# Performance work log

Hardware: AMD Instinct MI355X
Metric: run time of the kernel (lower is better)

Reference implementation:

```python
import jax, jax.numpy as jnp
import numpy as np

B, S, D, H = 4, 2048, 768, 12
HD = D // H  # 64


def setup_inputs() -> dict:
    key = jax.random.key(0)
    ks = jax.random.split(key, 6)
    sc = 0.02
    return {
        "x": jax.random.normal(ks[0], (B, S, D), dtype=jnp.float32),
        "wq": jax.random.normal(ks[1], (D, D), dtype=jnp.float32) * sc,
        "wk": jax.random.normal(ks[2], (D, D), dtype=jnp.float32) * sc,
        "wv": jax.random.normal(ks[3], (D, D), dtype=jnp.float32) * sc,
        "wo": jax.random.normal(ks[4], (D, D), dtype=jnp.float32) * sc,
        "bo": jnp.zeros((D,), dtype=jnp.float32),
    }


def reference(x, wq, wk, wv, wo, bo):
    b, s, d = x.shape
    # nn.Linear applies x @ W^T; project then split heads -> [b, h, s, hd]
    def heads(w):
        return (x @ w.T).reshape(b, s, H, HD).transpose(0, 2, 1, 3)
    q, k, v = heads(wq), heads(wk), heads(wv)
    scores = jnp.einsum("bhqd,bhkd->bhqk", q, k)
    causal = jnp.triu(jnp.ones((s, s), dtype=bool), 1)
    # original masks with -inf BEFORE scaling; -inf/sqrt(d) == -inf, same softmax
    scores = jnp.where(causal, -jnp.inf, scores) / jnp.sqrt(jnp.float32(HD))
    attn = jax.nn.softmax(scores, axis=-1)  # dropout=0.0 (eval/deterministic)
    ctx = jnp.einsum("bhqk,bhkd->bhqd", attn, v)
    ctx = ctx.transpose(0, 2, 1, 3).reshape(b, s, d)
    return ctx @ wo.T + bo
```

## Files before the change

kernel.cpp:

```cpp
#include <hip/hip_runtime.h>

#define B_ 4
#define S_ 2048
#define D_ 768
#define H_ 12
#define HD_ 64
#define T_ (B_ * S_)

typedef __bf16 bf16x8 __attribute__((ext_vector_type(8)));
typedef __bf16 bf16x4 __attribute__((ext_vector_type(4)));
typedef float  f32x4  __attribute__((ext_vector_type(4)));

__device__ __forceinline__ f32x4 mfma16(bf16x8 a, bf16x8 b, f32x4 c) {
  return __builtin_amdgcn_mfma_f32_16x16x32_bf16(a, b, c, 0, 0, 0);
}

__device__ __forceinline__ float fexp2(float x) {
  float r;
  asm("v_exp_f32 %0, %1" : "=v"(r) : "v"(x));
  return r;
}

__device__ __forceinline__ void gload16(const __bf16* g, __bf16* lds) {
  __builtin_amdgcn_global_load_lds(
      (__attribute__((address_space(1))) void*)g,
      (__attribute__((address_space(3))) void*)lds, 16, 0, 0);
}

__global__ void cvt_all(const float* __restrict__ x,
                        const float* __restrict__ wq,
                        const float* __restrict__ wk,
                        const float* __restrict__ wv,
                        const float* __restrict__ wo,
                        __bf16* __restrict__ out) {
  constexpr int XN4 = T_ * D_ / 4;
  constexpr int WN4 = D_ * D_ / 4;
  const int i = blockIdx.x * blockDim.x + threadIdx.x;
  if (i >= XN4 + 4 * WN4) return;
  const float* src;
  int k;
  float scale = 1.0f;
  if (i < XN4) {
    src = x;
    k = i;
  } else {
    const int j = i - XN4;
    const int wsel = j / WN4;
    k = j - wsel * WN4;
    src = (wsel == 0) ? wq : (wsel == 1) ? wk : (wsel == 2) ? wv : wo;
    if (wsel == 1) scale = 0.18033688f;
  }
  const float4 v = reinterpret_cast<const float4*>(src)[k];
  bf16x4 o;
  o[0] = (__bf16)(v.x * scale);
  o[1] = (__bf16)(v.y * scale);
  o[2] = (__bf16)(v.z * scale);
  o[3] = (__bf16)(v.w * scale);
  reinterpret_cast<bf16x4*>(out)[i] = o;
}

template <int MODE>
__global__ __launch_bounds__(256)
__attribute__((amdgpu_waves_per_eu(2)))
void gemm_bt(const __bf16* __restrict__ A,
             const __bf16* __restrict__ W0, const __bf16* __restrict__ W1,
             const __bf16* __restrict__ W2,
             __bf16* __restrict__ Oq, __bf16* __restrict__ Ok,
             __bf16* __restrict__ Ov,
             float* __restrict__ fout, const float* __restrict__ bias) {
  constexpr int K = D_;
  constexpr int NT = K / 64;
  __shared__ __align__(16) char smem[65536];
  __bf16* sA0 = reinterpret_cast<__bf16*>(smem);
  __bf16* sB0 = reinterpret_cast<__bf16*>(smem + 32768);

  const int tid = threadIdx.x;
  const int l = tid & 63;
  const int w = tid >> 6;

  const int flat = blockIdx.y * 64 + blockIdx.x;
  const int xcd = flat & 7;
  const int q = flat >> 3;
  const int mtile = xcd * 8 + (q & 7);
  const int pan = q >> 3;
  const int m0 = mtile * 128;

  int mat, n0;
  const __bf16* Wm;
  if (MODE == 0) {
    mat = pan / 6;
    n0 = (pan % 6) * 128;
    Wm = (mat == 0) ? W0 : (mat == 1) ? W1 : W2;
  } else {
    mat = 0;
    n0 = pan * 128;
    Wm = W0;
  }

  const int srow = l >> 3;
  const int scol = ((l & 7) ^ srow) * 8;
  const __bf16* gA[4];
  const __bf16* gB[4];
#pragma unroll
  for (int i = 0; i < 4; ++i) {
    const int c = w * 4 + i;
    gA[i] = A + (size_t)(m0 + c * 8 + srow) * K + scol;
    gB[i] = Wm + (size_t)(n0 + c * 8 + srow) * K + scol;
  }

  f32x4 acc[4][4] = {};
  const int wr = w >> 1, wc = w & 1;
  const int fr = l & 15, fq = l >> 4;
  const int swz = (fr & 7) << 4;

#pragma unroll
  for (int i = 0; i < 4; ++i) {
    const int c = w * 4 + i;
    gload16(gA[i], &sA0[c * 512]);
    gload16(gB[i], &sB0[c * 512]);
  }
#pragma unroll
  for (int i = 0; i < 4; ++i) {
    const int c = w * 4 + i;
    gload16(gA[i] + 64, &sA0[8192 + c * 512]);
    gload16(gB[i] + 64, &sB0[8192 + c * 512]);
  }

  int cur = 0;
  for (int kt = 0; kt < NT; ++kt) {
    if (kt + 1 < NT)
      asm volatile("s_waitcnt vmcnt(8)" ::: "memory");
    else
      asm volatile("s_waitcnt vmcnt(0)" ::: "memory");
    __builtin_amdgcn_s_barrier();

    const char* ab = reinterpret_cast<const char*>(&sA0[cur * 8192]);
    const char* bb = reinterpret_cast<const char*>(&sB0[cur * 8192]);
#pragma unroll
    for (int ks = 0; ks < 2; ++ks) {
      bf16x8 af[4], bfr[4];
#pragma unroll
      for (int mi = 0; mi < 4; ++mi)
        af[mi] = *reinterpret_cast<const bf16x8*>(
            ab + (wr * 64 + mi * 16 + fr) * 128 +
            ((ks * 64 + fq * 16) ^ swz));
#pragma unroll
      for (int ni = 0; ni < 4; ++ni)
        bfr[ni] = *reinterpret_cast<const bf16x8*>(
            bb + (wc * 64 + ni * 16 + fr) * 128 +
            ((ks * 64 + fq * 16) ^ swz));
#pragma unroll
      for (int mi = 0; mi < 4; ++mi)
#pragma unroll
        for (int ni = 0; ni < 4; ++ni)
          acc[mi][ni] = mfma16(af[mi], bfr[ni], acc[mi][ni]);
    }
    __builtin_amdgcn_s_barrier();

    if (kt + 2 < NT) {
      const int ko = (kt + 2) * 64;
#pragma unroll
      for (int i = 0; i < 4; ++i) {
        const int c = w * 4 + i;
        gload16(gA[i] + ko, &sA0[cur * 8192 + c * 512]);
        gload16(gB[i] + ko, &sB0[cur * 8192 + c * 512]);
      }
    }
    cur ^= 1;
  }

  if (MODE == 0 && mat == 2) {
#pragma unroll
    for (int mi = 0; mi < 4; ++mi) {
      const int mbase = m0 + wr * 64 + mi * 16 + fq * 4;
      const int b = mbase >> 11, s = mbase & (S_ - 1);
#pragma unroll
      for (int ni = 0; ni < 4; ++ni) {
        const int o = n0 + wc * 64 + ni * 16 + fr;
        const int h = o >> 6, hd = o & 63;
        bf16x4 vv;
#pragma unroll
        for (int r = 0; r < 4; ++r) vv[r] = (__bf16)acc[mi][ni][r];
        *reinterpret_cast<bf16x4*>(
            &Ov[((size_t)((b * H_ + h) * HD_ + hd)) * S_ + s]) = vv;
      }
    }
  } else {
    float* fW = reinterpret_cast<float*>(smem) + w * 4096;
#pragma unroll
    for (int mi = 0; mi < 4; ++mi)
#pragma unroll
      for (int ni = 0; ni < 4; ++ni)
#pragma unroll
        for (int r = 0; r < 4; ++r)
          fW[(mi * 16 + fq * 4 + r) * 64 + ni * 16 + fr] = acc[mi][ni][r];
    if (MODE == 1) {
      const int ocol = n0 + wc * 64 + fr * 4;
      const float4 bs = *reinterpret_cast<const float4*>(&bias[ocol]);
#pragma unroll
      for (int it = 0; it < 16; ++it) {
        const int lrow = it * 4 + fq;
        f32x4 v = *reinterpret_cast<const f32x4*>(&fW[lrow * 64 + fr * 4]);
        v[0] += bs.x;
        v[1] += bs.y;
        v[2] += bs.z;
        v[3] += bs.w;
        *reinterpret_cast<f32x4*>(
            &fout[(size_t)(m0 + wr * 64 + lrow) * D_ + ocol]) = v;
      }
    } else {
      const int o = n0 + wc * 64;
      const int h = o >> 6;
      __bf16* dst = (mat == 0) ? Oq : Ok;
#pragma unroll
      for (int it = 0; it < 16; ++it) {
        const int lrow = it * 4 + fq;
        const int m = m0 + wr * 64 + lrow;
        const int b = m >> 11, s = m & (S_ - 1);
        const f32x4 v =
            *reinterpret_cast<const f32x4*>(&fW[lrow * 64 + fr * 4]);
        bf16x4 ov;
#pragma unroll
        for (int r = 0; r < 4; ++r) ov[r] = (__bf16)v[r];
        *reinterpret_cast<bf16x4*>(
            &dst[((size_t)((b * H_ + h) * S_ + s)) * HD_ + fr * 4]) = ov;
      }
    }
  }
}

__global__ __launch_bounds__(256)
__attribute__((amdgpu_waves_per_eu(5)))
void attn_kernel(const __bf16* __restrict__ Q, const __bf16* __restrict__ Kt,
                 const __bf16* __restrict__ Vt, __bf16* __restrict__ C) {
  __shared__ __align__(16) __bf16 sK[2][64 * 64];
  __shared__ __align__(16) __bf16 sV[64 * 64];
  __shared__ __align__(16) __bf16 sP[4][16 * 64];

  const int tid = threadIdx.x;
  const int l = tid & 63;
  const int w = tid >> 6;
  const int fr = l & 15, fq = l >> 4;
  const int bx = blockIdx.x;
  const int xcd = bx & 7;
  const int j = bx >> 3;
  const int bh = xcd + 8 * (j % 6);
  const int qtile = 31 - j / 6;
  const int qb = qtile * 64;
  const int qbw = qb + w * 16;

  const __bf16* qh = Q + (size_t)bh * S_ * HD_;
  const __bf16* kh = Kt + (size_t)bh * S_ * HD_;
  const __bf16* vh = Vt + (size_t)bh * HD_ * S_;
  char* sPb = reinterpret_cast<char*>(&sP[w][0]);

  const int srow = l >> 3;
  const int scol = ((l & 7) * 8) ^ (srow << 3);
  const int swz = (fr & 7) << 4;

  bf16x8 qf[2];
#pragma unroll
  for (int ks = 0; ks < 2; ++ks)
    qf[ks] = *reinterpret_cast<const bf16x8*>(
        &qh[(size_t)(qbw + fr) * HD_ + ks * 32 + fq * 8]);

  f32x4 acc[4] = {};
  float mrow = -1e30f, lrow = 0.f;

  const int nt = qtile + 1;
  int cur = 0;
  const int q0 = 2 * w, q1 = 2 * w + 1;

  gload16(kh + (size_t)(q0 * 8 + srow) * HD_ + scol, &sK[0][q0 * 512]);
  gload16(kh + (size_t)(q1 * 8 + srow) * HD_ + scol, &sK[0][q1 * 512]);
  gload16(vh + (size_t)(q0 * 8 + srow) * S_ + scol, &sV[q0 * 512]);
  gload16(vh + (size_t)(q1 * 8 + srow) * S_ + scol, &sV[q1 * 512]);
  if (nt > 1) {
    gload16(kh + (size_t)(64 + q0 * 8 + srow) * HD_ + scol, &sK[1][q0 * 512]);
    gload16(kh + (size_t)(64 + q1 * 8 + srow) * HD_ + scol, &sK[1][q1 * 512]);
  }

  for (int t = 0; t < nt; ++t) {
    if (t + 1 < nt)
      asm volatile("s_waitcnt vmcnt(2)" ::: "memory");
    else
      asm volatile("s_waitcnt vmcnt(0)" ::: "memory");
    __builtin_amdgcn_s_barrier();

    const int kv0 = t * 64;
    if (kv0 <= qbw + 15) {
      const char* kb = reinterpret_cast<const char*>(&sK[cur][0]);
      const char* vb = reinterpret_cast<const char*>(&sV[0]);

      f32x4 s[4];
      __builtin_amdgcn_s_setprio(1);
#pragma unroll
      for (int c = 0; c < 4; ++c) {
        const int row = c * 16 + fr;
        bf16x8 kf0 = *reinterpret_cast<const bf16x8*>(
            kb + row * 128 + ((fq * 16) ^ swz));
        bf16x8 kf1 = *reinterpret_cast<const bf16x8*>(
            kb + row * 128 + ((fq * 16 + 64) ^ swz));
        f32x4 z = {};
        z = mfma16(kf0, qf[0], z);
        z = mfma16(kf1, qf[1], z);
        s[c] = z;
      }
      __builtin_amdgcn_s_setprio(0);

      if (kv0 + 63 > qbw) {
        const int qi = qbw + fr;
#pragma unroll
        for (int c = 0; c < 4; ++c)
#pragma unroll
          for (int r = 0; r < 4; ++r) {
            const int kvi = kv0 + c * 16 + fq * 4 + r;
            if (kvi > qi) s[c][r] = -1e30f;
          }
      }

      float tm = -1e30f;
#pragma unroll
      for (int c = 0; c < 4; ++c)
#pragma unroll
        for (int r = 0; r < 4; ++r) tm = fmaxf(tm, s[c][r]);
      tm = fmaxf(tm, __shfl_xor(tm, 16));
      tm = fmaxf(tm, __shfl_xor(tm, 32));
      const bool defer = __all(tm - mrow <= 8.0f);
      const float mn = defer ? mrow : fmaxf(mrow, tm);
      if (!defer) {
        const float fac = fexp2(mrow - mn);
        mrow = mn;
        lrow *= fac;
#pragma unroll
        for (int dt = 0; dt < 4; ++dt)
#pragma unroll
          for (int r = 0; r < 4; ++r) acc[dt][r] *= fac;
      }
      float sum = 0.f;
#pragma unroll
      for (int c = 0; c < 4; ++c) {
        bf16x4 pc;
#pragma unroll
        for (int r = 0; r < 4; ++r) {
          const float p = fexp2(s[c][r] - mn);
          sum += p;
          pc[r] = (__bf16)p;
        }
        const int bo = (c * 32 + fq * 8) ^ swz;
        *reinterpret_cast<bf16x4*>(sPb + fr * 128 + bo) = pc;
      }
      lrow += sum;

      bf16x8 pa[2];
#pragma unroll
      for (int ks = 0; ks < 2; ++ks) {
        const int bo = (ks * 64 + fq * 16) ^ swz;
        pa[ks] = *reinterpret_cast<const bf16x8*>(sPb + fr * 128 + bo);
      }

      __builtin_amdgcn_s_setprio(1);
#pragma unroll
      for (int dt = 0; dt < 4; ++dt) {
        const int row = dt * 16 + fr;
        bf16x8 vf0 = *reinterpret_cast<const bf16x8*>(
            vb + row * 128 + ((fq * 16) ^ swz));
        bf16x8 vf1 = *reinterpret_cast<const bf16x8*>(
            vb + row * 128 + ((fq * 16 + 64) ^ swz));
        acc[dt] = mfma16(vf0, pa[0], acc[dt]);
        acc[dt] = mfma16(vf1, pa[1], acc[dt]);
      }
      __builtin_amdgcn_s_setprio(0);
    }

    __builtin_amdgcn_s_barrier();

    if (t + 1 < nt) {
      const int kvn = (t + 1) * 64;
      gload16(vh + (size_t)(q0 * 8 + srow) * S_ + kvn + scol, &sV[q0 * 512]);
      gload16(vh + (size_t)(q1 * 8 + srow) * S_ + kvn + scol, &sV[q1 * 512]);
    }
    if (t + 2 < nt) {
      const int kvn = (t + 2) * 64;
      gload16(kh + (size_t)(kvn + q0 * 8 + srow) * HD_ + scol,
              &sK[cur][q0 * 512]);
      gload16(kh + (size_t)(kvn + q1 * 8 + srow) * HD_ + scol,
              &sK[cur][q1 * 512]);
    }
    cur ^= 1;
  }

  float lt = lrow;
  lt += __shfl_xor(lt, 16);
  lt += __shfl_xor(lt, 32);
  const int b = bh / H_, h = bh % H_;
  const float inv_l = 1.0f / lt;
  const int qrow = qbw + fr;
#pragma unroll
  for (int dt = 0; dt < 4; ++dt) {
    bf16x4 ov;
#pragma unroll
    for (int r = 0; r < 4; ++r) ov[r] = (__bf16)(acc[dt][r] * inv_l);
    *reinterpret_cast<bf16x4*>(
        &C[((size_t)(b * S_ + qrow)) * D_ + h * HD_ + dt * 16 + fq * 4]) = ov;
  }
}

static constexpr size_t XB_OFF = 0;
static constexpr size_t WQ_OFF = XB_OFF + (size_t)T_ * D_;
static constexpr size_t WK_OFF = WQ_OFF + (size_t)D_ * D_;
static constexpr size_t WV_OFF = WK_OFF + (size_t)D_ * D_;
static constexpr size_t WO_OFF = WV_OFF + (size_t)D_ * D_;
static constexpr size_t Q_OFF = WO_OFF + (size_t)D_ * D_;
static constexpr size_t K_OFF = Q_OFF + (size_t)T_ * D_;
static constexpr size_t V_OFF = K_OFF + (size_t)T_ * D_;
static constexpr size_t C_OFF = V_OFF + (size_t)T_ * D_;

extern "C" void kernel_launch(void* const* d_in, const int* in_sizes, int n_in,
                              void* d_out, int out_size, void* d_ws,
                              size_t ws_size, hipStream_t stream) {
  const float* x = (const float*)d_in[0];
  const float* wq = (const float*)d_in[1];
  const float* wk = (const float*)d_in[2];
  const float* wv = (const float*)d_in[3];
  const float* wo = (const float*)d_in[4];
  const float* bo = (const float*)d_in[5];
  float* out = (float*)d_out;
  __bf16* ws = (__bf16*)d_ws;

  __bf16* xb = ws + XB_OFF;
  __bf16* wqb = ws + WQ_OFF;
  __bf16* wkb = ws + WK_OFF;
  __bf16* wvb = ws + WV_OFF;
  __bf16* wob = ws + WO_OFF;
  __bf16* qbuf = ws + Q_OFF;
  __bf16* kbuf = ws + K_OFF;
  __bf16* vbuf = ws + V_OFF;
  __bf16* cbuf = ws + C_OFF;

  {
    constexpr int n4 = T_ * D_ / 4 + 4 * (D_ * D_ / 4);
    cvt_all<<<(n4 + 255) / 256, 256, 0, stream>>>(x, wq, wk, wv, wo, ws);
  }

  gemm_bt<0><<<dim3(64, 18), 256, 0, stream>>>(
      xb, wqb, wkb, wvb, qbuf, kbuf, vbuf, nullptr, nullptr);

  attn_kernel<<<dim3(1536), 256, 0, stream>>>(qbuf, kbuf, vbuf, cbuf);

  gemm_bt<1><<<dim3(64, 6), 256, 0, stream>>>(
      cbuf, wob, nullptr, nullptr, nullptr, nullptr, nullptr, out, bo);
}
```

Measured before the change: 115.3 us.

## Cut GEMM LDS to 48KB by single-buffering B tile for higher occupancy

The GEMM kernel now double-buffers only the A tile and keeps a single B buffer, loaded for the next k-step right after the compute barrier. The epilogue stages accumulators through LDS in two halves so it fits the smaller 48KB allocation. Waves per EU are raised from 2 to 3 so more blocks can be resident and hide latency. The trade-off is that B loads now have only the barrier-to-next-iteration window to land, which can expose memory latency.

```diff
diff --git a/kernel.cpp b/kernel.cpp
--- a/kernel.cpp
+++ b/kernel.cpp
@@ -61,7 +61,7 @@
 
 template <int MODE>
 __global__ __launch_bounds__(256)
-__attribute__((amdgpu_waves_per_eu(2)))
+__attribute__((amdgpu_waves_per_eu(3)))
 void gemm_bt(const __bf16* __restrict__ A,
              const __bf16* __restrict__ W0, const __bf16* __restrict__ W1,
              const __bf16* __restrict__ W2,
@@ -70,7 +70,7 @@
              float* __restrict__ fout, const float* __restrict__ bias) {
   constexpr int K = D_;
   constexpr int NT = K / 64;
-  __shared__ __align__(16) char smem[65536];
+  __shared__ __align__(16) char smem[49152];
   __bf16* sA0 = reinterpret_cast<__bf16*>(smem);
   __bf16* sB0 = reinterpret_cast<__bf16*>(smem + 32768);
 
@@ -114,28 +114,23 @@
   const int swz = (fr & 7) << 4;
 
 #pragma unroll
-  for (int i = 0; i < 4; ++i) {
-    const int c = w * 4 + i;
-    gload16(gA[i], &sA0[c * 512]);
-    gload16(gB[i], &sB0[c * 512]);
-  }
-#pragma unroll
-  for (int i = 0; i < 4; ++i) {
-    const int c = w * 4 + i;
-    gload16(gA[i] + 64, &sA0[8192 + c * 512]);
-    gload16(gB[i] + 64, &sB0[8192 + c * 512]);
-  }
+  for (int i = 0; i < 4; ++i) gload16(gA[i], &sA0[(w * 4 + i) * 512]);
+#pragma unroll
+  for (int i = 0; i < 4; ++i) gload16(gB[i], &sB0[(w * 4 + i) * 512]);
+#pragma unroll
+  for (int i = 0; i < 4; ++i)
+    gload16(gA[i] + 64, &sA0[8192 + (w * 4 + i) * 512]);
 
   int cur = 0;
   for (int kt = 0; kt < NT; ++kt) {
     if (kt + 1 < NT)
-      asm volatile("s_waitcnt vmcnt(8)" ::: "memory");
+      asm volatile("s_waitcnt vmcnt(4)" ::: "memory");
     else
       asm volatile("s_waitcnt vmcnt(0)" ::: "memory");
     __builtin_amdgcn_s_barrier();
 
     const char* ab = reinterpret_cast<const char*>(&sA0[cur * 8192]);
-    const char* bb = reinterpret_cast<const char*>(&sB0[cur * 8192]);
+    const char* bb = reinterpret_cast<const char*>(sB0);
 #pragma unroll
     for (int ks = 0; ks < 2; ++ks) {
       bf16x8 af[4], bfr[4];
@@ -157,14 +152,17 @@
     }
     __builtin_amdgcn_s_barrier();
 
+    if (kt + 1 < NT) {
+      const int ko = (kt + 1) * 64;
+#pragma unroll
+      for (int i = 0; i < 4; ++i)
+        gload16(gB[i] + ko, &sB0[(w * 4 + i) * 512]);
+    }
     if (kt + 2 < NT) {
       const int ko = (kt + 2) * 64;
 #pragma unroll
-      for (int i = 0; i < 4; ++i) {
-        const int c = w * 4 + i;
-        gload16(gA[i] + ko, &sA0[cur * 8192 + c * 512]);
-        gload16(gB[i] + ko, &sB0[cur * 8192 + c * 512]);
-      }
+      for (int i = 0; i < 4; ++i)
+        gload16(gA[i] + ko, &sA0[cur * 8192 + (w * 4 + i) * 512]);
     }
     cur ^= 1;
   }
@@ -186,44 +184,49 @@
       }
     }
   } else {
-    float* fW = reinterpret_cast<float*>(smem) + w * 4096;
-#pragma unroll
-    for (int mi = 0; mi < 4; ++mi)
-#pragma unroll
-      for (int ni = 0; ni < 4; ++ni)
-#pragma unroll
-        for (int r = 0; r < 4; ++r)
-          fW[(mi * 16 + fq * 4 + r) * 64 + ni * 16 + fr] = acc[mi][ni][r];
-    if (MODE == 1) {
-      const int ocol = n0 + wc * 64 + fr * 4;
-      const float4 bs = *reinterpret_cast<const float4*>(&bias[ocol]);
-#pragma unroll
-      for (int it = 0; it < 16; ++it) {
-        const int lrow = it * 4 + fq;
-        f32x4 v = *reinterpret_cast<const f32x4*>(&fW[lrow * 64 + fr * 4]);
-        v[0] += bs.x;
-        v[1] += bs.y;
-        v[2] += bs.z;
-        v[3] += bs.w;
-        *reinterpret_cast<f32x4*>(
-            &fout[(size_t)(m0 + wr * 64 + lrow) * D_ + ocol]) = v;
-      }
-    } else {
-      const int o = n0 + wc * 64;
-      const int h = o >> 6;
-      __bf16* dst = (mat == 0) ? Oq : Ok;
-#pragma unroll
-      for (int it = 0; it < 16; ++it) {
-        const int lrow = it * 4 + fq;
-        const int m = m0 + wr * 64 + lrow;
-        const int b = m >> 11, s = m & (S_ - 1);
-        const f32x4 v =
-            *reinterpret_cast<const f32x4*>(&fW[lrow * 64 + fr * 4]);
-        bf16x4 ov;
-#pragma unroll
-        for (int r = 0; r < 4; ++r) ov[r] = (__bf16)v[r];
-        *reinterpret_cast<bf16x4*>(
-            &dst[((size_t)((b * H_ + h) * S_ + s)) * HD_ + fr * 4]) = ov;
+    float* fW = reinterpret_cast<float*>(smem) + w * 2048;
+#pragma unroll
+    for (int half = 0; half < 2; ++half) {
+#pragma unroll
+      for (int mi2 = 0; mi2 < 2; ++mi2)
+#pragma unroll
+        for (int ni = 0; ni < 4; ++ni)
+#pragma unroll
+          for (int r = 0; r < 4; ++r)
+            fW[(mi2 * 16 + fq * 4 + r) * 64 + ni * 16 + fr] =
+                acc[half * 2 + mi2][ni][r];
+      if (MODE == 1) {
+        const int ocol = n0 + wc * 64 + fr * 4;
+        const float4 bs = *reinterpret_cast<const float4*>(&bias[ocol]);
+#pragma unroll
+        for (int it = 0; it < 8; ++it) {
+          const int lrow = it * 4 + fq;
+          f32x4 v = *reinterpret_cast<const f32x4*>(&fW[lrow * 64 + fr * 4]);
+          v[0] += bs.x;
+          v[1] += bs.y;
+          v[2] += bs.z;
+          v[3] += bs.w;
+          *reinterpret_cast<f32x4*>(
+              &fout[(size_t)(m0 + wr * 64 + half * 32 + lrow) * D_ + ocol]) =
+              v;
+        }
+      } else {
+        const int o = n0 + wc * 64;
+        const int h = o >> 6;
+        __bf16* dst = (mat == 0) ? Oq : Ok;
+#pragma unroll
+        for (int it = 0; it < 8; ++it) {
+          const int lrow = it * 4 + fq;
+          const int m = m0 + wr * 64 + half * 32 + lrow;
+          const int b = m >> 11, s = m & (S_ - 1);
+          const f32x4 v =
+              *reinterpret_cast<const f32x4*>(&fW[lrow * 64 + fr * 4]);
+          bf16x4 ov;
+#pragma unroll
+          for (int r = 0; r < 4; ++r) ov[r] = (__bf16)v[r];
+          *reinterpret_cast<bf16x4*>(
+              &dst[((size_t)((b * H_ + h) * S_ + s)) * HD_ + fr * 4]) = ov;
+        }
       }
     }
   }
```

After: 114.6 us. No clear change (-0.6%).
